# Performance work log

Hardware: AMD Instinct MI355X
Metric: run time of the kernel (lower is better)

The kernel has to match this reference:

```python
import jax, jax.numpy as jnp
import numpy as np

TIME_UNITS = 10.0
EPS_LN = 1e-5
N_NODES, N_EDGES, BATCH, T_IN = 20000, 320000, 8, 12
H_PROB, H_VEL = 64, 32


def _layernorm(x, g, b):
    mu = jnp.mean(x, axis=-1, keepdims=True)
    var = jnp.mean((x - mu) ** 2, axis=-1, keepdims=True)
    return (x - mu) / jnp.sqrt(var + EPS_LN) * g + b


def setup_inputs() -> dict:
    key = jax.random.key(0)
    ks = jax.random.split(key, 20)
    s = 0.1
    inp = {}
    inp['upstream'] = jax.random.uniform(ks[0], (N_EDGES, BATCH, T_IN), jnp.float32)
    inp['downstream'] = jax.random.uniform(ks[1], (N_EDGES, BATCH, T_IN), jnp.float32)
    inp['feature'] = jax.random.uniform(ks[2], (N_NODES, BATCH, T_IN), jnp.float32)
    inp['distance'] = jax.random.uniform(ks[3], (N_EDGES,), jnp.float32, 10.0, 500.0)
    inp['src'] = jax.random.randint(ks[4], (N_EDGES,), 0, N_NODES, jnp.int32)
    inp['dst'] = jax.random.randint(ks[5], (N_EDGES,), 0, N_NODES, jnp.int32)
    inp['fc_w'] = jax.random.normal(ks[6], (H_PROB, T_IN), jnp.float32) * s
    inp['attn_w'] = jax.random.normal(ks[7], (1, 2 * H_PROB + 1), jnp.float32) * s
    inp['ln2_g'] = jnp.ones((2 * H_PROB + 1,), jnp.float32)
    inp['ln2_b'] = jnp.zeros((2 * H_PROB + 1,), jnp.float32)
    inp['v11_w'] = jax.random.normal(ks[8], (H_VEL, T_IN), jnp.float32) * s
    inp['v11_b'] = jnp.zeros((H_VEL,), jnp.float32)
    inp['ln11_g'] = jnp.ones((H_VEL,), jnp.float32)
    inp['ln11_b'] = jnp.zeros((H_VEL,), jnp.float32)
    inp['v12_w'] = jax.random.normal(ks[9], (1, H_VEL), jnp.float32) * s
    inp['v12_b'] = jnp.zeros((1,), jnp.float32)
    inp['v21_w'] = jax.random.normal(ks[10], (H_VEL, T_IN), jnp.float32) * s
    inp['v21_b'] = jnp.zeros((H_VEL,), jnp.float32)
    inp['ln21_g'] = jnp.ones((H_VEL,), jnp.float32)
    inp['ln21_b'] = jnp.zeros((H_VEL,), jnp.float32)
    inp['v22_w'] = jax.random.normal(ks[11], (1, H_VEL), jnp.float32) * s
    inp['v22_b'] = jnp.zeros((1,), jnp.float32)
    inp['v3_w'] = jax.random.normal(ks[12], (1, 2), jnp.float32) * s
    inp['v3_b'] = jnp.zeros((1,), jnp.float32)
    inp['alpha'] = jnp.ones((N_EDGES, 1), jnp.float32)
    return inp


def reference(upstream, downstream, feature, distance, src, dst,
              fc_w, attn_w, ln2_g, ln2_b,
              v11_w, v11_b, ln11_g, ln11_b, v12_w, v12_b,
              v21_w, v21_b, ln21_g, ln21_b, v22_w, v22_b,
              v3_w, v3_b, alpha):
    N, B, T = feature.shape
    Tf = jnp.asarray(T, feature.dtype)

    # --- Velocity_Model_NAM (eval mode: dropout = identity) ---
    def branch(x, w1, b1, g, bn, w2, b2):
        h = jax.nn.relu(_layernorm(x @ w1.T + b1, g, bn))
        return jax.nn.sigmoid(h @ w2.T + b2)  # [E,B,1]

    xu = branch(upstream, v11_w, v11_b, ln11_g, ln11_b, v12_w, v12_b)
    xd = branch(downstream, v21_w, v21_b, ln21_g, ln21_b, v22_w, v22_b)
    v = jnp.log1p(jnp.exp((jnp.concatenate([xu, xd], -1) @ v3_w.T + v3_b)[..., 0]))  # [E,B]

    # --- per-edge travel time and diffusion kernel ---
    Tt = distance[:, None] / (v + 1e-5)                # [E,B]
    T_idx = jnp.round(Tt / TIME_UNITS)
    T_idx = jnp.where(T_idx < 0, 0.0, T_idx)
    T_idx = jnp.where(T_idx > Tf, Tf - 1.0, T_idx)     # strictly > T_in, as in masked_fill
    F = 1.0 / (1.0 + alpha * Tt)                       # [E,B]
    n = jnp.maximum(Tf - T_idx, 1.0)                   # sequence length per (edge,batch)
    t = jnp.arange(T, dtype=feature.dtype)
    mask = t < n[..., None]
    expo = jnp.maximum(n[..., None] - 1.0 - t, 0.0)    # decreasing exponents n-1..0
    diffusion = jnp.where(mask, F[..., None] * jnp.power(1.0 - F[..., None], expo), 0.0)  # [E,B,T]

    # --- Probabilistic_Model: embeddings + edge softmax normalized per SOURCE node ---
    z = feature @ fc_w.T                               # [N,B,64]
    zc = jnp.concatenate([z[src], z[dst], jax.lax.stop_gradient(v)[..., None]], -1)  # [E,B,129]
    a = jax.nn.leaky_relu((_layernorm(zc, ln2_g, ln2_b) @ attn_w.T)[..., 0], 0.01)   # [E,B]
    m = jax.ops.segment_max(a, src, num_segments=N)
    ex = jnp.exp(a - m[src])
    den = jax.ops.segment_sum(ex, src, num_segments=N)
    score = ex / den[src]

    # --- mailbox reduce: attention-weighted diffusion prediction per destination ---
    pred_edge = jnp.sum(diffusion * feature[src], -1)  # [E,B]
    pred = jax.ops.segment_sum(score * pred_edge, dst, num_segments=N)  # [N,B]
    return pred
```

## Files before the change

### kernel.cpp

```cpp
#include <hip/hip_runtime.h>
#include <math.h>

#define TB 8
#define TT 12
#define HV 32

typedef float v2f __attribute__((ext_vector_type(2)));

#define PK_B1 384
#define PK_TL 416
#define PK_STRIDE 576

__device__ __forceinline__ float vel_branch32(const v2f xv[6], const float* swb, float b2) {
  v2f h2[16];
  v2f s1v = {0.f, 0.f}, s2v = {0.f, 0.f};
#pragma unroll
  for (int jp = 0; jp < 16; ++jp) {
    const float4* wr = (const float4*)(swb + jp * 24);
    float4 a0 = wr[0], a1 = wr[1], a2 = wr[2];
    float4 c0 = wr[3], c1 = wr[4], c2 = wr[5];
    v2f bj = *(const v2f*)(swb + PK_B1 + 2*jp);
    v2f p0 = xv[0] * (v2f){a0.x, a0.y};
    p0 = __builtin_elementwise_fma(xv[1], (v2f){a0.z, a0.w}, p0);
    p0 = __builtin_elementwise_fma(xv[2], (v2f){a1.x, a1.y}, p0);
    p0 = __builtin_elementwise_fma(xv[3], (v2f){a1.z, a1.w}, p0);
    p0 = __builtin_elementwise_fma(xv[4], (v2f){a2.x, a2.y}, p0);
    p0 = __builtin_elementwise_fma(xv[5], (v2f){a2.z, a2.w}, p0);
    v2f p1 = xv[0] * (v2f){c0.x, c0.y};
    p1 = __builtin_elementwise_fma(xv[1], (v2f){c0.z, c0.w}, p1);
    p1 = __builtin_elementwise_fma(xv[2], (v2f){c1.x, c1.y}, p1);
    p1 = __builtin_elementwise_fma(xv[3], (v2f){c1.z, c1.w}, p1);
    p1 = __builtin_elementwise_fma(xv[4], (v2f){c2.x, c2.y}, p1);
    p1 = __builtin_elementwise_fma(xv[5], (v2f){c2.z, c2.w}, p1);
    v2f hv = { p0.x + p0.y + bj.x, p1.x + p1.y + bj.y };
    h2[jp] = hv;
    s1v += hv;
    s2v = __builtin_elementwise_fma(hv, hv, s2v);
  }
  float s1 = s1v.x + s1v.y;
  float s2 = s2v.x + s2v.y;
  float mu  = s1 * (1.f/HV);
  float var = s2 * (1.f/HV) - mu*mu;
  float inv = 1.f / sqrtf(var + 1e-5f);
  v2f mu2  = {mu, mu};
  v2f inv2 = {inv, inv};
  v2f zero = {0.f, 0.f};
  v2f acc2 = {b2, 0.f};
#pragma unroll
  for (int jp = 0; jp < 16; ++jp) {
    float4 t0 = *(const float4*)(swb + PK_TL + 8*jp);
    v2f w2v   = *(const v2f*)(swb + PK_TL + 8*jp + 4);
    v2f gv  = {t0.x, t0.y};
    v2f bnv = {t0.z, t0.w};
    v2f yl = __builtin_elementwise_fma((h2[jp] - mu2) * inv2, gv, bnv);
    yl = __builtin_elementwise_max(yl, zero);
    acc2 = __builtin_elementwise_fma(yl, w2v, acc2);
  }
  return 1.f / (1.f + __expf(-(acc2.x + acc2.y)));
}

__device__ double vel_branch64(const float* x,
    const float* __restrict__ w1, const float* __restrict__ b1,
    const float* __restrict__ g,  const float* __restrict__ bn,
    const float* __restrict__ w2, float b2) {
  double s1 = 0.0, s2 = 0.0;
  for (int j = 0; j < HV; ++j) {
    double hj = (double)b1[j];
    for (int t = 0; t < TT; ++t) hj = fma((double)x[t], (double)w1[j*TT+t], hj);
    s1 += hj;
    s2 = fma(hj, hj, s2);
  }
  double mu  = s1 / (double)HV;
  double var = s2 / (double)HV - mu*mu;
  double inv = 1.0 / sqrt(var + 1e-5);
  double acc = (double)b2;
  for (int j = 0; j < HV; ++j) {
    double hj = (double)b1[j];
    for (int t = 0; t < TT; ++t) hj = fma((double)x[t], (double)w1[j*TT+t], hj);
    double yl = (hj - mu) * inv * (double)g[j] + (double)bn[j];
    if (yl < 0.0) yl = 0.0;
    acc = fma(yl, (double)w2[j], acc);
  }
  return 1.0 / (1.0 + exp(-acc));
}

__global__ void __launch_bounds__(256) k_prep(
    float* __restrict__ den, float* __restrict__ pred, int nb,
    const float* __restrict__ attn_w, const float* __restrict__ ln2_g,
    const float* __restrict__ ln2_b,
    const float* __restrict__ v11_w, const float* __restrict__ v11_b,
    const float* __restrict__ ln11_g, const float* __restrict__ ln11_b,
    const float* __restrict__ v12_w, const float* __restrict__ v12_b,
    const float* __restrict__ v21_w, const float* __restrict__ v21_b,
    const float* __restrict__ ln21_g, const float* __restrict__ ln21_b,
    const float* __restrict__ v22_w, const float* __restrict__ v22_b,
    const float* __restrict__ v3_w, const float* __restrict__ v3_b,
    float* __restrict__ scal, float* __restrict__ pack, int* __restrict__ fixcnt) {
  int idx = blockIdx.x * blockDim.x + threadIdx.x;
  for (int i = idx; i < nb; i += gridDim.x * blockDim.x) { den[i] = 0.f; pred[i] = 0.f; }
  if (blockIdx.x == 0) {
    __shared__ float sg[256], sb[256];
    float a = 0.f, b = 0.f;
    if (threadIdx.x < 129) {
      float w = attn_w[threadIdx.x];
      a = w * ln2_g[threadIdx.x];
      b = w * ln2_b[threadIdx.x];
    }
    sg[threadIdx.x] = a; sb[threadIdx.x] = b;
    __syncthreads();
    for (int s = 128; s > 0; s >>= 1) {
      if (threadIdx.x < s) { sg[threadIdx.x] += sg[threadIdx.x+s]; sb[threadIdx.x] += sb[threadIdx.x+s]; }
      __syncthreads();
    }
    if (threadIdx.x == 0) {
      scal[0] = sg[0]; scal[1] = sb[0];
      scal[2] = attn_w[128] * ln2_g[128];
      scal[3] = v12_b[0];  scal[4] = v22_b[0];
      scal[5] = v3_w[0];   scal[6] = v3_w[1];  scal[7] = v3_b[0];
      fixcnt[0] = 0;
    }
  } else if (blockIdx.x <= 2) {
    int br = blockIdx.x - 1;
    const float* W1 = br ? v21_w : v11_w;
    const float* B1 = br ? v21_b : v11_b;
    const float* G  = br ? ln21_g : ln11_g;
    const float* BN = br ? ln21_b : ln11_b;
    const float* W2 = br ? v22_w : v12_w;
    float* p = pack + br * PK_STRIDE;
    for (int i = threadIdx.x; i < PK_STRIDE; i += 256) {
      float val = 0.f;
      if (i < PK_B1)      val = W1[i];
      else if (i < PK_TL) val = B1[i - PK_B1];
      else if (i < 544) {
        int q = i - PK_TL, jp = q >> 3, k = q & 7;
        int j = 2*jp + (k & 1);
        if (k < 2)      val = G[j];
        else if (k < 4) val = BN[j];
        else if (k < 6) val = W2[j];
      }
      p[i] = val;
    }
  }
}

__global__ void __launch_bounds__(256, 2) k_node(
    const float* __restrict__ feature, const float* __restrict__ fc_w,
    const float* __restrict__ attn_w,  const float* __restrict__ ln2_g,
    float4* __restrict__ nodepre, int n_nodes) {
  int idx = blockIdx.x * blockDim.x + threadIdx.x;
  int total = n_nodes * TB;
  if (idx >= total) return;
  const float4* f4 = (const float4*)(feature + (size_t)idx * TT);
  float4 fa = f4[0], fb = f4[1], fcv = f4[2];
  v2f xv[6] = {{fa.x,fa.y},{fa.z,fa.w},{fb.x,fb.y},{fb.z,fb.w},{fcv.x,fcv.y},{fcv.z,fcv.w}};
  float q = 0.f, r = 0.f, ps = 0.f, pd = 0.f;
#pragma unroll 8
  for (int i = 0; i < 64; ++i) {
    v2f p = {0.f, 0.f};
#pragma unroll
    for (int k = 0; k < 6; ++k)
      p = __builtin_elementwise_fma(xv[k], *(const v2f*)(fc_w + i*TT + 2*k), p);
    float z = p.x + p.y;
    q += z;
    r  = fmaf(z, z, r);
    ps = fmaf(z, attn_w[i]      * ln2_g[i],      ps);
    pd = fmaf(z, attn_w[64 + i] * ln2_g[64 + i], pd);
  }
  nodepre[idx] = make_float4(q, r, ps, pd);
}

__global__ void __launch_bounds__(256, 2) k_edge1(
    const float* __restrict__ upstream, const float* __restrict__ downstream,
    const float* __restrict__ feature,  const float* __restrict__ distance,
    const int* __restrict__ src, const int* __restrict__ dst,
    const float* __restrict__ alpha,
    const float* __restrict__ pack,
    const float4* __restrict__ nodepre, const float* __restrict__ scal,
    float2* __restrict__ epbuf, float* __restrict__ den,
    int* __restrict__ fixcnt, int* __restrict__ fixlist, int fixcap,
    int n_edges) {
  __shared__ float sw[2 * PK_STRIDE];
  for (int i = threadIdx.x; i < 2 * PK_STRIDE / 4; i += 256)
    ((float4*)sw)[i] = ((const float4*)pack)[i];
  __syncthreads();

  int idx = blockIdx.x * blockDim.x + threadIdx.x;
  if (idx >= n_edges * TB) return;
  int e = idx >> 3, b = idx & 7;

  float sc0 = scal[0], sc1 = scal[1], aw128 = scal[2];
  float b2u = scal[3], b2d = scal[4];
  float w3a = scal[5], w3b = scal[6], b3 = scal[7];

  int s = src[e], d = dst[e];
  float dist = distance[e];
  float al   = alpha[e];
  const float4* f4 = (const float4*)(feature + ((size_t)s * TB + b) * TT);
  float4 f0 = f4[0], f1 = f4[1], f2 = f4[2];
  float4 nps = nodepre[(size_t)s * TB + b];
  float4 npd = nodepre[(size_t)d * TB + b];

  float xu, xd;
  {
    const float4* u4 = (const float4*)(upstream + (size_t)idx * TT);
    float4 a0 = u4[0], a1 = u4[1], a2 = u4[2];
    v2f xv[6] = {{a0.x,a0.y},{a0.z,a0.w},{a1.x,a1.y},{a1.z,a1.w},{a2.x,a2.y},{a2.z,a2.w}};
    xu = vel_branch32(xv, sw, b2u);
  }
  {
    const float4* d4 = (const float4*)(downstream + (size_t)idx * TT);
    float4 c0 = d4[0], c1 = d4[1], c2 = d4[2];
    v2f xv[6] = {{c0.x,c0.y},{c0.z,c0.w},{c1.x,c1.y},{c1.z,c1.w},{c2.x,c2.y},{c2.z,c2.w}};
    xd = vel_branch32(xv, sw + PK_STRIDE, b2d);
  }
  float y = fmaf(xu, w3a, fmaf(xd, w3b, b3));
  float v = fmaxf(y, 0.f) + __logf(1.f + __expf(-fabsf(y)));

  float tt  = dist / (v + 1e-5f);
  float th  = tt * 0.1f;
  float tif = rintf(th);

  float frac = th - tif;
  if (fabsf(fabsf(frac) - 0.5f) < 2.5e-4f && th < 11.0f) {
    int p = atomicAdd(fixcnt, 1);
    if (p < fixcap) fixlist[p] = idx;
  }

  int ti = (int)tif;
  ti = ti < 0 ? 0 : (ti > TT ? TT - 1 : ti);
  int n = TT - ti; n = n < 1 ? 1 : n;

  float F  = 1.f / fmaf(al, tt, 1.f);
  float om = 1.f - F;

  float feat[TT] = {f0.x,f0.y,f0.z,f0.w, f1.x,f1.y,f1.z,f1.w, f2.x,f2.y,f2.z,f2.w};
  float acc = 0.f;
#pragma unroll
  for (int t = 0; t < TT; ++t) {
    acc = (t < n) ? fmaf(acc, om, feat[t]) : acc;
  }
  float pe = F * acc;

  float sum   = nps.x + npd.x + v;
  float sumsq = nps.y + npd.y + v*v;
  float mu  = sum * (1.f/129.f);
  float var = sumsq * (1.f/129.f) - mu*mu;
  float S1  = nps.z + npd.w + v * aw128;
  float aa  = (S1 - mu*sc0) / sqrtf(var + 1e-5f) + sc1;
  float a   = aa >= 0.f ? aa : 0.01f*aa;
  float ex  = __expf(a);

  epbuf[idx] = make_float2(ex, pe);
  atomicAdd(&den[s * TB + b], ex);
}

__global__ void __launch_bounds__(256) k_fix(
    const float* __restrict__ upstream, const float* __restrict__ downstream,
    const float* __restrict__ feature,  const float* __restrict__ distance,
    const int* __restrict__ src, const int* __restrict__ dst,
    const float* __restrict__ v11_w, const float* __restrict__ v11_b,
    const float* __restrict__ ln11_g, const float* __restrict__ ln11_b,
    const float* __restrict__ v12_w, const float* __restrict__ v12_b,
    const float* __restrict__ v21_w, const float* __restrict__ v21_b,
    const float* __restrict__ ln21_g, const float* __restrict__ ln21_b,
    const float* __restrict__ v22_w, const float* __restrict__ v22_b,
    const float* __restrict__ v3_w, const float* __restrict__ v3_b,
    const float* __restrict__ alpha,
    const float4* __restrict__ nodepre, const float* __restrict__ scal,
    float2* __restrict__ epbuf, float* __restrict__ den,
    const int* __restrict__ fixcnt, const int* __restrict__ fixlist, int fixcap) {
  int cnt = fixcnt[0];
  if (cnt > fixcap) cnt = fixcap;
  int stride = gridDim.x * blockDim.x;
  for (int i = blockIdx.x * blockDim.x + threadIdx.x; i < cnt; i += stride) {
    int idx = fixlist[i];
    int e = idx >> 3, b = idx & 7;
    int s = src[e], d = dst[e];
    float dist = distance[e];
    float al   = alpha[e];

    const float* xr_u = upstream   + (size_t)idx * TT;
    const float* xr_d = downstream + (size_t)idx * TT;
    double xu64 = vel_branch64(xr_u, v11_w, v11_b, ln11_g, ln11_b, v12_w, v12_b[0]);
    double xd64 = vel_branch64(xr_d, v21_w, v21_b, ln21_g, ln21_b, v22_w, v22_b[0]);
    double y64  = xu64*(double)v3_w[0] + xd64*(double)v3_w[1] + (double)v3_b[0];
    double v64  = log1p(exp(y64));
    double tt64 = (double)dist / (v64 + 1e-5);
    float v   = (float)v64;
    float tt  = (float)tt64;
    float tif = (float)rint(tt64 * 0.1);

    int ti = (int)tif;
    ti = ti < 0 ? 0 : (ti > TT ? TT - 1 : ti);
    int n = TT - ti; n = n < 1 ? 1 : n;

    float F  = 1.f / fmaf(al, tt, 1.f);
    float om = 1.f - F;

    const float* feat = feature + ((size_t)s * TB + b) * TT;
    float acc = 0.f;
    for (int t = 0; t < n; ++t) acc = fmaf(acc, om, feat[t]);
    float pe = F * acc;

    float4 nps = nodepre[(size_t)s * TB + b];
    float4 npd = nodepre[(size_t)d * TB + b];
    float sum   = nps.x + npd.x + v;
    float sumsq = nps.y + npd.y + v*v;
    float mu  = sum * (1.f/129.f);
    float var = sumsq * (1.f/129.f) - mu*mu;
    float S1  = nps.z + npd.w + v * scal[2];
    float aa  = (S1 - mu*scal[0]) / sqrtf(var + 1e-5f) + scal[1];
    float a   = aa >= 0.f ? aa : 0.01f*aa;
    float ex  = __expf(a);

    float2 old = epbuf[idx];
    epbuf[idx] = make_float2(ex, pe);
    atomicAdd(&den[s * TB + b], ex - old.x);
  }
}

__global__ void __launch_bounds__(256) k_edge2(
    const int* __restrict__ src, const int* __restrict__ dst,
    const float2* __restrict__ epbuf,
    const float* __restrict__ den, float* __restrict__ pred, int n_edges) {
  int idx = blockIdx.x * blockDim.x + threadIdx.x;
  if (idx >= n_edges * TB) return;
  int e = idx >> 3, b = idx & 7;
  float2 ep = epbuf[idx];
  float score = ep.x / den[src[e] * TB + b];
  atomicAdd(&pred[dst[e] * TB + b], score * ep.y);
}

extern "C" void kernel_launch(void* const* d_in, const int* in_sizes, int n_in,
                              void* d_out, int out_size, void* d_ws, size_t ws_size,
                              hipStream_t stream) {
  const float* upstream   = (const float*)d_in[0];
  const float* downstream = (const float*)d_in[1];
  const float* feature    = (const float*)d_in[2];
  const float* distance   = (const float*)d_in[3];
  const int*   src        = (const int*)d_in[4];
  const int*   dst        = (const int*)d_in[5];
  const float* fc_w   = (const float*)d_in[6];
  const float* attn_w = (const float*)d_in[7];
  const float* ln2_g  = (const float*)d_in[8];
  const float* ln2_b  = (const float*)d_in[9];
  const float* v11_w  = (const float*)d_in[10];
  const float* v11_b  = (const float*)d_in[11];
  const float* ln11_g = (const float*)d_in[12];
  const float* ln11_b = (const float*)d_in[13];
  const float* v12_w  = (const float*)d_in[14];
  const float* v12_b  = (const float*)d_in[15];
  const float* v21_w  = (const float*)d_in[16];
  const float* v21_b  = (const float*)d_in[17];
  const float* ln21_g = (const float*)d_in[18];
  const float* ln21_b = (const float*)d_in[19];
  const float* v22_w  = (const float*)d_in[20];
  const float* v22_b  = (const float*)d_in[21];
  const float* v3_w   = (const float*)d_in[22];
  const float* v3_b   = (const float*)d_in[23];
  const float* alpha  = (const float*)d_in[24];

  int E  = in_sizes[4];
  int N  = in_sizes[2] / (TB * TT);
  int NB = N * TB;
  int EB = E * TB;
  int fixcap = EB / 8;

  float*  ws      = (float*)d_ws;
  float4* nodepre = (float4*)ws;
  float2* epbuf   = (float2*)(ws + 4 * (size_t)NB);
  float*  den     = ws + 4 * (size_t)NB + 2 * (size_t)EB;
  float*  scal    = den + NB;
  float*  pack    = scal + 8;
  int*    fixcnt  = (int*)(pack + 2 * PK_STRIDE);
  int*    fixlist = fixcnt + 4;
  float*  pred    = (float*)d_out;

  int blk = 256;
  k_prep<<<(NB + blk - 1) / blk, blk, 0, stream>>>(
      den, pred, NB, attn_w, ln2_g, ln2_b,
      v11_w, v11_b, ln11_g, ln11_b, v12_w, v12_b,
      v21_w, v21_b, ln21_g, ln21_b, v22_w, v22_b,
      v3_w, v3_b, scal, pack, fixcnt);
  k_node<<<(NB + blk - 1) / blk, blk, 0, stream>>>(feature, fc_w, attn_w, ln2_g, nodepre, N);
  k_edge1<<<(EB + blk - 1) / blk, blk, 0, stream>>>(
      upstream, downstream, feature, distance, src, dst, alpha,
      pack, nodepre, scal, epbuf, den, fixcnt, fixlist, fixcap, E);
  k_fix<<<16, blk, 0, stream>>>(
      upstream, downstream, feature, distance, src, dst,
      v11_w, v11_b, ln11_g, ln11_b, v12_w, v12_b,
      v21_w, v21_b, ln21_g, ln21_b, v22_w, v22_b,
      v3_w, v3_b, alpha,
      nodepre, scal, epbuf, den, fixcnt, fixlist, fixcap);
  k_edge2<<<(EB + blk - 1) / blk, blk, 0, stream>>>(src, dst, epbuf, den, pred, E);
}
```

Measured before the change: 171.0 us.

## Fuse prep into node kernel, transpose velocity MLP weights, pair edge2 work

Merges the prep kernel into the node kernel, removing one launch. The packed velocity weights are transposed to a t-major layout, and the first layer becomes an outer-product accumulation; the LayerNorm mean now comes from precomputed column sums of W1 and the bias sum rather than a running sum. k_edge2 now has each thread handle two batch entries using vector loads of epbuf and den. Risks: the k_node and k_edge1 dependency on pack and scal within the fused kernel is fine because k_edge1 is a separate launch, and the mean computed via column sums may differ slightly numerically.

Result: slower. 186.4 us (+9.0%).

```diff
diff --git a/kernel.cpp b/kernel.cpp
--- a/kernel.cpp
+++ b/kernel.cpp
@@ -7,38 +7,43 @@
 
 typedef float v2f __attribute__((ext_vector_type(2)));
 
-#define PK_B1 384
-#define PK_TL 416
+#define PK_B1  384
+#define PK_TL  416
+#define PK_CS  544
+#define PK_SB1 556
 #define PK_STRIDE 576
 
 __device__ __forceinline__ float vel_branch32(const v2f xv[6], const float* swb, float b2) {
   v2f h2[16];
-  v2f s1v = {0.f, 0.f}, s2v = {0.f, 0.f};
-#pragma unroll
-  for (int jp = 0; jp < 16; ++jp) {
-    const float4* wr = (const float4*)(swb + jp * 24);
-    float4 a0 = wr[0], a1 = wr[1], a2 = wr[2];
-    float4 c0 = wr[3], c1 = wr[4], c2 = wr[5];
-    v2f bj = *(const v2f*)(swb + PK_B1 + 2*jp);
-    v2f p0 = xv[0] * (v2f){a0.x, a0.y};
-    p0 = __builtin_elementwise_fma(xv[1], (v2f){a0.z, a0.w}, p0);
-    p0 = __builtin_elementwise_fma(xv[2], (v2f){a1.x, a1.y}, p0);
-    p0 = __builtin_elementwise_fma(xv[3], (v2f){a1.z, a1.w}, p0);
-    p0 = __builtin_elementwise_fma(xv[4], (v2f){a2.x, a2.y}, p0);
-    p0 = __builtin_elementwise_fma(xv[5], (v2f){a2.z, a2.w}, p0);
-    v2f p1 = xv[0] * (v2f){c0.x, c0.y};
-    p1 = __builtin_elementwise_fma(xv[1], (v2f){c0.z, c0.w}, p1);
-    p1 = __builtin_elementwise_fma(xv[2], (v2f){c1.x, c1.y}, p1);
-    p1 = __builtin_elementwise_fma(xv[3], (v2f){c1.z, c1.w}, p1);
-    p1 = __builtin_elementwise_fma(xv[4], (v2f){c2.x, c2.y}, p1);
-    p1 = __builtin_elementwise_fma(xv[5], (v2f){c2.z, c2.w}, p1);
-    v2f hv = { p0.x + p0.y + bj.x, p1.x + p1.y + bj.y };
-    h2[jp] = hv;
-    s1v += hv;
-    s2v = __builtin_elementwise_fma(hv, hv, s2v);
-  }
-  float s1 = s1v.x + s1v.y;
+#pragma unroll
+  for (int q = 0; q < 8; ++q) {
+    float4 b4 = *(const float4*)(swb + PK_B1 + 4*q);
+    h2[2*q]   = (v2f){b4.x, b4.y};
+    h2[2*q+1] = (v2f){b4.z, b4.w};
+  }
+#pragma unroll
+  for (int t = 0; t < TT; ++t) {
+    float xs = xv[t>>1][t&1];
+    v2f xb = {xs, xs};
+    const float* wr = swb + t*32;
+#pragma unroll
+    for (int q = 0; q < 8; ++q) {
+      float4 w4 = *(const float4*)(wr + 4*q);
+      h2[2*q]   = __builtin_elementwise_fma(xb, (v2f){w4.x, w4.y}, h2[2*q]);
+      h2[2*q+1] = __builtin_elementwise_fma(xb, (v2f){w4.z, w4.w}, h2[2*q+1]);
+    }
+  }
+  v2f s1p = {swb[PK_SB1], 0.f};
+#pragma unroll
+  for (int k = 0; k < 6; ++k)
+    s1p = __builtin_elementwise_fma(xv[k], *(const v2f*)(swb + PK_CS + 2*k), s1p);
+  float s1 = s1p.x + s1p.y;
+  v2f s2v = h2[0] * h2[0];
+#pragma unroll
+  for (int jp = 1; jp < 16; ++jp)
+    s2v = __builtin_elementwise_fma(h2[jp], h2[jp], s2v);
   float s2 = s2v.x + s2v.y;
+
   float mu  = s1 * (1.f/HV);
   float var = s2 * (1.f/HV) - mu*mu;
   float inv = 1.f / sqrtf(var + 1e-5f);
@@ -84,9 +89,9 @@
   return 1.0 / (1.0 + exp(-acc));
 }
 
-__global__ void __launch_bounds__(256) k_prep(
-    float* __restrict__ den, float* __restrict__ pred, int nb,
-    const float* __restrict__ attn_w, const float* __restrict__ ln2_g,
+__global__ void __launch_bounds__(256, 2) k_node(
+    const float* __restrict__ feature, const float* __restrict__ fc_w,
+    const float* __restrict__ attn_w,  const float* __restrict__ ln2_g,
     const float* __restrict__ ln2_b,
     const float* __restrict__ v11_w, const float* __restrict__ v11_b,
     const float* __restrict__ ln11_g, const float* __restrict__ ln11_b,
@@ -95,9 +100,12 @@
     const float* __restrict__ ln21_g, const float* __restrict__ ln21_b,
     const float* __restrict__ v22_w, const float* __restrict__ v22_b,
     const float* __restrict__ v3_w, const float* __restrict__ v3_b,
-    float* __restrict__ scal, float* __restrict__ pack, int* __restrict__ fixcnt) {
+    float4* __restrict__ nodepre, float* __restrict__ den, float* __restrict__ pred,
+    float* __restrict__ scal, float* __restrict__ pack, int* __restrict__ fixcnt,
+    int nb) {
   int idx = blockIdx.x * blockDim.x + threadIdx.x;
-  for (int i = idx; i < nb; i += gridDim.x * blockDim.x) { den[i] = 0.f; pred[i] = 0.f; }
+  if (idx < nb) { den[idx] = 0.f; pred[idx] = 0.f; }
+
   if (blockIdx.x == 0) {
     __shared__ float sg[256], sb[256];
     float a = 0.f, b = 0.f;
@@ -129,27 +137,32 @@
     float* p = pack + br * PK_STRIDE;
     for (int i = threadIdx.x; i < PK_STRIDE; i += 256) {
       float val = 0.f;
-      if (i < PK_B1)      val = W1[i];
-      else if (i < PK_TL) val = B1[i - PK_B1];
-      else if (i < 544) {
+      if (i < PK_B1) {
+        int t = i >> 5, j = i & 31;
+        val = W1[j*TT + t];
+      } else if (i < PK_TL) {
+        val = B1[i - PK_B1];
+      } else if (i < PK_CS) {
         int q = i - PK_TL, jp = q >> 3, k = q & 7;
         int j = 2*jp + (k & 1);
         if (k < 2)      val = G[j];
         else if (k < 4) val = BN[j];
         else if (k < 6) val = W2[j];
+      } else if (i < PK_SB1) {
+        int t = i - PK_CS;
+        float cs = 0.f;
+        for (int j = 0; j < HV; ++j) cs += W1[j*TT + t];
+        val = cs;
+      } else if (i == PK_SB1) {
+        float sb1 = 0.f;
+        for (int j = 0; j < HV; ++j) sb1 += B1[j];
+        val = sb1;
       }
       p[i] = val;
     }
   }
-}
-
-__global__ void __launch_bounds__(256, 2) k_node(
-    const float* __restrict__ feature, const float* __restrict__ fc_w,
-    const float* __restrict__ attn_w,  const float* __restrict__ ln2_g,
-    float4* __restrict__ nodepre, int n_nodes) {
-  int idx = blockIdx.x * blockDim.x + threadIdx.x;
-  int total = n_nodes * TB;
-  if (idx >= total) return;
+
+  if (idx >= nb) return;
   const float4* f4 = (const float4*)(feature + (size_t)idx * TT);
   float4 fa = f4[0], fb = f4[1], fcv = f4[2];
   v2f xv[6] = {{fa.x,fa.y},{fa.z,fa.w},{fb.x,fb.y},{fb.z,fb.w},{fcv.x,fcv.y},{fcv.z,fcv.w}};
@@ -322,13 +335,16 @@
 __global__ void __launch_bounds__(256) k_edge2(
     const int* __restrict__ src, const int* __restrict__ dst,
     const float2* __restrict__ epbuf,
-    const float* __restrict__ den, float* __restrict__ pred, int n_edges) {
+    const float* __restrict__ den, float* __restrict__ pred, int n_pairs) {
   int idx = blockIdx.x * blockDim.x + threadIdx.x;
-  if (idx >= n_edges * TB) return;
-  int e = idx >> 3, b = idx & 7;
-  float2 ep = epbuf[idx];
-  float score = ep.x / den[src[e] * TB + b];
-  atomicAdd(&pred[dst[e] * TB + b], score * ep.y);
+  if (idx >= n_pairs) return;
+  int row0 = idx * 2;
+  int e = row0 >> 3, b0 = row0 & 7;
+  float4 ep = ((const float4*)epbuf)[idx];
+  int s = src[e], d = dst[e];
+  float2 dn = *(const float2*)(den + s * TB + b0);
+  atomicAdd(&pred[d * TB + b0],     (ep.x / dn.x) * ep.y);
+  atomicAdd(&pred[d * TB + b0 + 1], (ep.z / dn.y) * ep.w);
 }
 
 extern "C" void kernel_launch(void* const* d_in, const int* in_sizes, int n_in,
@@ -377,12 +393,12 @@
   float*  pred    = (float*)d_out;
 
   int blk = 256;
-  k_prep<<<(NB + blk - 1) / blk, blk, 0, stream>>>(
-      den, pred, NB, attn_w, ln2_g, ln2_b,
+  k_node<<<(NB + blk - 1) / blk, blk, 0, stream>>>(
+      feature, fc_w, attn_w, ln2_g, ln2_b,
       v11_w, v11_b, ln11_g, ln11_b, v12_w, v12_b,
       v21_w, v21_b, ln21_g, ln21_b, v22_w, v22_b,
-      v3_w, v3_b, scal, pack, fixcnt);
-  k_node<<<(NB + blk - 1) / blk, blk, 0, stream>>>(feature, fc_w, attn_w, ln2_g, nodepre, N);
+      v3_w, v3_b,
+      nodepre, den, pred, scal, pack, fixcnt, NB);
   k_edge1<<<(EB + blk - 1) / blk, blk, 0, stream>>>(
       upstream, downstream, feature, distance, src, dst, alpha,
       pack, nodepre, scal, epbuf, den, fixcnt, fixlist, fixcap, E);
@@ -392,5 +408,5 @@
       v21_w, v21_b, ln21_g, ln21_b, v22_w, v22_b,
       v3_w, v3_b, alpha,
       nodepre, scal, epbuf, den, fixcnt, fixlist, fixcap);
-  k_edge2<<<(EB + blk - 1) / blk, blk, 0, stream>>>(src, dst, epbuf, den, pred, E);
-}
+  k_edge2<<<(EB / 2 + blk - 1) / blk, blk, 0, stream>>>(src, dst, epbuf, den, pred, EB / 2);
+}
```
